# Kernel optimization log

Measured on AMD Instinct MI355X. Metric: run time of the kernel, lower is better.

Reference implementation:

```python
import jax, jax.numpy as jnp
import numpy as np
import math

D_MODEL = 1024
NUM_HEADS = 16
HEAD_DIM = D_MODEL // NUM_HEADS
THETA = 10000.0
B, S = 2, 2048


def _rope(x, positions, theta):
    # x: (b, h, s, d); positions: (s,) int
    d = x.shape[-1]
    inv_freq = theta ** (-jnp.arange(0, d, 2, dtype=jnp.float32) / d)  # (d/2,)
    ang = positions.astype(jnp.float32)[:, None] * inv_freq[None, :]   # (s, d/2)
    cos, sin = jnp.cos(ang), jnp.sin(ang)
    x1 = x[..., ::2]
    x2 = x[..., 1::2]
    r1 = x1 * cos - x2 * sin
    r2 = x1 * sin + x2 * cos
    # interleave back to (..., d)
    return jnp.stack([r1, r2], axis=-1).reshape(x.shape)


def setup_inputs() -> dict:
    key = jax.random.key(0)
    ks = jax.random.split(key, 5)
    std = math.sqrt(2.0 / (D_MODEL + D_MODEL))
    return {
        "x": jax.random.normal(ks[0], (B, S, D_MODEL), dtype=jnp.float32),
        "token_positions": jnp.arange(S, dtype=jnp.int32),
        "Wq": jax.random.normal(ks[1], (D_MODEL, D_MODEL), dtype=jnp.float32) * std,
        "Wk": jax.random.normal(ks[2], (D_MODEL, D_MODEL), dtype=jnp.float32) * std,
        "Wv": jax.random.normal(ks[3], (D_MODEL, D_MODEL), dtype=jnp.float32) * std,
        "Wo": jax.random.normal(ks[4], (D_MODEL, D_MODEL), dtype=jnp.float32) * std,
    }


def reference(x, token_positions, Wq, Wk, Wv, Wo):
    b, s, _ = x.shape
    def split_heads(t):
        return t.reshape(b, s, NUM_HEADS, HEAD_DIM).transpose(0, 2, 1, 3)  # (b,h,s,d)
    Q = split_heads(x @ Wq.T)
    K = split_heads(x @ Wk.T)
    V = split_heads(x @ Wv.T)
    Q = _rope(Q, token_positions, THETA)
    K = _rope(K, token_positions, THETA)
    scores = jnp.einsum("bhqd,bhkd->bhqk", Q, K) / math.sqrt(HEAD_DIM)
    causal = jnp.tril(jnp.ones((s, s), dtype=bool))
    scores = jnp.where(causal, scores, -jnp.inf)
    attn = jax.nn.softmax(scores, axis=-1)
    out = jnp.einsum("bhqk,bhkd->bhqd", attn, V)
    out = out.transpose(0, 2, 1, 3).reshape(b, s, D_MODEL)
    return out @ Wo.T
```

## Files before the change

kernel.cpp:

```cpp
#include <hip/hip_runtime.h>
#include <math.h>

typedef unsigned short u16;
typedef unsigned int   u32;
typedef __attribute__((ext_vector_type(8))) short bf16x8;
typedef __attribute__((ext_vector_type(4))) float floatx4;
typedef __attribute__((ext_vector_type(4))) _Float16 halfx4;
typedef __attribute__((ext_vector_type(2))) unsigned int uintx2;

#define SEQ 2048
#define DM  1024
#define NH  16
#define DH  64
#define MM  4096
#define QSCALE 0.18033688011112042f

__device__ __forceinline__ u16 f2bf(float f) {
    u32 u = __builtin_bit_cast(u32, f);
    u += 0x7fffu + ((u >> 16) & 1u);
    return (u16)(u >> 16);
}

__device__ __forceinline__ void async16(const void* g, void* l) {
    __builtin_amdgcn_global_load_lds(
        (const __attribute__((address_space(1))) void*)g,
        (__attribute__((address_space(3))) void*)l, 16, 0, 0);
}

__global__ __launch_bounds__(256) void prep_kernel(const float* __restrict__ x,
                                                   const float* __restrict__ w0,
                                                   const float* __restrict__ w1,
                                                   const float* __restrict__ w2,
                                                   const float* __restrict__ w3,
                                                   u16* __restrict__ Xsh,
                                                   u16* __restrict__ Wsh,
                                                   const int* __restrict__ pos,
                                                   float2* __restrict__ tab) {
    const int bid = blockIdx.x, cb = blockIdx.y, tid = threadIdx.x;

    int lin = bid * 16 + cb;
    if (lin < 256) {
        int i = lin * 256 + tid;
        int p = i >> 5, d2 = i & 31;
        float freq = __expf(-(float)d2 * (9.2103403719761836f / 32.0f));
        float sv, cv;
        sincosf((float)pos[p] * freq, &sv, &cv);
        tab[i] = make_float2(cv, sv);
    }

    const float* src; u16* dst; int row0;
    if (bid < 64) { src = x; dst = Xsh; row0 = bid * 64; }
    else {
        int wi = (bid - 64) >> 4;
        src = (wi == 0) ? w0 : (wi == 1) ? w1 : (wi == 2) ? w2 : w3;
        dst = Wsh + (size_t)wi * DM * DM;
        row0 = ((bid - 64) & 15) * 64;
    }
    __shared__ __align__(16) u16 t[64 * 64];
#pragma unroll
    for (int rep = 0; rep < 4; ++rep) {
        int f = rep * 256 + tid;
        int r = f >> 4, c4 = f & 15;
        float4 v = *(const float4*)&src[(size_t)(row0 + r) * DM + cb * 64 + c4 * 4];
        uint2 pk;
        pk.x = (u32)f2bf(v.x) | ((u32)f2bf(v.y) << 16);
        pk.y = (u32)f2bf(v.z) | ((u32)f2bf(v.w) << 16);
        int ch = (c4 >> 1) ^ (r & 7);
        *(uint2*)&t[r * 64 + ch * 8 + (c4 & 1) * 4] = pk;
    }
    __syncthreads();
#pragma unroll
    for (int rep = 0; rep < 2; ++rep) {
        int s = rep * 256 + tid;
        int tile = s >> 6, l = s & 63;
        int mt = tile >> 1, kt = tile & 1, lm = l & 15, quad = l >> 4;
        int m = mt * 16 + lm;
        uint4 v = *(const uint4*)&t[m * 64 + ((kt * 4 + quad) ^ (m & 7)) * 8];
        size_t rowblk = (size_t)(row0 >> 4) + mt;
        size_t ktile  = cb * 2 + kt;
        *(uint4*)&dst[(rowblk * 32 + ktile) * 512 + l * 8] = v;
    }
}

template<int NZ, bool OUTF32>
__global__ __launch_bounds__(256, 2) void gemm_f(const u16* __restrict__ Ash,
                                                 const u16* __restrict__ Wbase,
                                                 u16* __restrict__ outbf,
                                                 float* __restrict__ outf,
                                                 _Float16* __restrict__ vtout,
                                                 u16* __restrict__ koutbf,
                                                 const float2* __restrict__ ropetab) {
    const int m0 = blockIdx.x * 64, n0 = blockIdx.y * 128;
    const int tid = threadIdx.x, lane = tid & 63, w = tid >> 6;
    const int lm = lane & 15, quad = lane >> 4;
    const int rb0 = m0 >> 4;
    const int cb0 = n0 >> 4;

    __shared__ __align__(16) u16 lsA[2][4 * 512];
    __shared__ __align__(16) u16 lsB[2][NZ * 8 * 512];

    const u16* aSrc = Ash + ((size_t)(rb0 + w) * 32) * 512 + lane * 8;
    constexpr int NPW = NZ * 2;
    const u16* bSrc[NPW];
#pragma unroll
    for (int j = 0; j < NPW; ++j) {
        int p = w * NPW + j, z = p >> 3, cb8 = p & 7;
        bSrc[j] = Wbase + (size_t)z * (DM * DM)
                + ((size_t)(cb0 + cb8) * 32) * 512 + lane * 8;
    }

    auto stage = [&](int buf, int it) {
        async16(aSrc + (size_t)it * 512, &lsA[buf][w * 512 + lane * 8]);
#pragma unroll
        for (int j = 0; j < NPW; ++j)
            async16(bSrc[j] + (size_t)it * 512,
                    &lsB[buf][(w * NPW + j) * 512 + lane * 8]);
    };

    floatx4 acc[NZ][4][2];
    const floatx4 z4 = {0.f, 0.f, 0.f, 0.f};
#pragma unroll
    for (int z = 0; z < NZ; ++z)
#pragma unroll
        for (int mt = 0; mt < 4; ++mt)
#pragma unroll
            for (int nt = 0; nt < 2; ++nt) acc[z][mt][nt] = z4;

    stage(0, 0);
    __syncthreads();

#pragma unroll 2
    for (int it = 0; it < 32; ++it) {
        if (it < 31) stage((it + 1) & 1, it + 1);
        const u16* La = &lsA[it & 1][0];
        const u16* Lb = &lsB[it & 1][0];
        bf16x8 a[4], b[NZ][2];
#pragma unroll
        for (int mt = 0; mt < 4; ++mt)
            a[mt] = *(const bf16x8*)&La[mt * 512 + lane * 8];
#pragma unroll
        for (int z = 0; z < NZ; ++z)
#pragma unroll
            for (int nt = 0; nt < 2; ++nt)
                b[z][nt] = *(const bf16x8*)&Lb[(z * 8 + w * 2 + nt) * 512 + lane * 8];
#pragma unroll
        for (int z = 0; z < NZ; ++z)
#pragma unroll
            for (int mt = 0; mt < 4; ++mt)
#pragma unroll
                for (int nt = 0; nt < 2; ++nt)
                    acc[z][mt][nt] = __builtin_amdgcn_mfma_f32_16x16x32_bf16(
                        a[mt], b[z][nt], acc[z][mt][nt], 0, 0, 0);
        __syncthreads();
    }

#pragma unroll
    for (int z = 0; z < NZ; ++z) {
        if (!OUTF32 && NZ == 3 && z == 2) {
#pragma unroll
            for (int mt = 0; mt < 4; ++mt) {
                int row = m0 + mt * 16;
                int b = row >> 11;
                int sblk = (row & (SEQ - 1)) >> 4;
#pragma unroll
                for (int nt = 0; nt < 2; ++nt) {
                    int col = n0 + w * 32 + nt * 16;
                    int h = col >> 6;
                    int dblk = (col & 63) >> 4;
                    size_t chunk = ((size_t)(b * NH + h) * 128 + sblk) * 4 + dblk;
                    uint2 pk;
                    pk.x = __builtin_bit_cast(u32, __builtin_amdgcn_cvt_pkrtz(acc[z][mt][nt][0], acc[z][mt][nt][1]));
                    pk.y = __builtin_bit_cast(u32, __builtin_amdgcn_cvt_pkrtz(acc[z][mt][nt][2], acc[z][mt][nt][3]));
                    *(uint2*)&vtout[chunk * 256 + lane * 4] = pk;
                }
            }
            continue;
        }
        if (!OUTF32 && NZ == 3 && z == 1) {
            u16* t = (u16*)&lsB[0][0];
#pragma unroll
            for (int mt = 0; mt < 4; ++mt)
#pragma unroll
                for (int r = 0; r < 4; ++r) {
                    int row = m0 + mt * 16 + quad * 4 + r;
#pragma unroll
                    for (int nt = 0; nt < 2; ++nt) {
                        int col = n0 + w * 32 + nt * 16 + lm;
                        float v  = acc[z][mt][nt][r];
                        float pv = __shfl_xor(v, 1);
                        float2 cs = ropetab[(row & (SEQ - 1)) * 32 + ((col & 63) >> 1)];
                        v = (lm & 1) ? fmaf(pv, cs.y, v * cs.x) : fmaf(v, cs.x, -pv * cs.y);
                        t[(mt * 16 + quad * 4 + r) * 136 + (w * 32 + nt * 16 + lm)] = f2bf(v);
                    }
                }
            __syncthreads();
            {
                int bb = m0 >> 11;
                int sblk0 = (m0 & (SEQ - 1)) >> 4;
                int h0 = n0 >> 6;
#pragma unroll
                for (int j = 0; j < 4; ++j) {
                    int c = w * 4 + j;
                    int hloc = c >> 3, sblkl = (c >> 1) & 3, ks2 = c & 1;
                    uint4 v = *(const uint4*)&t[(sblkl * 16 + lm) * 136 + hloc * 64 + ks2 * 32 + quad * 8];
                    size_t chunk = ((size_t)(bb * NH + h0 + hloc) * 128 + sblk0 + sblkl) * 2 + ks2;
                    *(uint4*)&koutbf[chunk * 512 + lane * 8] = v;
                }
            }
            continue;
        }
        const bool rope = !OUTF32;
        const float osc = (!OUTF32 && z == 0) ? QSCALE : 1.0f;
#pragma unroll
        for (int mt = 0; mt < 4; ++mt)
#pragma unroll
            for (int r = 0; r < 4; ++r) {
                int row = m0 + mt * 16 + quad * 4 + r;
#pragma unroll
                for (int nt = 0; nt < 2; ++nt) {
                    int col = n0 + w * 32 + nt * 16 + lm;
                    float v  = acc[z][mt][nt][r];
                    if (rope) {
                        float pv = __shfl_xor(v, 1);
                        float2 cs = ropetab[(row & (SEQ - 1)) * 32 + ((col & 63) >> 1)];
                        v = (lm & 1) ? fmaf(pv, cs.y, v * cs.x) : fmaf(v, cs.x, -pv * cs.y);
                    }
                    v *= osc;
                    if (OUTF32) {
                        outf[(size_t)row * DM + col] = v;
                    } else {
                        float hv = __shfl_xor(v, 1);
                        if (!(lm & 1)) {
                            u32 pk = (u32)f2bf(v) | ((u32)f2bf(hv) << 16);
                            *(u32*)&outbf[(size_t)z * ((size_t)MM * DM) + (size_t)row * DM + col] = pk;
                        }
                    }
                }
            }
    }
}

__global__ __launch_bounds__(256, 2) void attn_kernel(const u16* __restrict__ Q,
                                                      const u16* __restrict__ Kf,
                                                      const _Float16* __restrict__ Vf,
                                                      u16* __restrict__ AO) {
    const int u  = blockIdx.x;
    const int qt = (u < 256) ? (15 - (u >> 5)) : ((u >> 5) - 8);
    const int bh = u & 31;
    const int b  = bh >> 4, h = bh & 15;
    const int q0 = qt * 128;
    const int tid = threadIdx.x, w = tid >> 6, lane = tid & 63;
    const int lm = lane & 15, quad = lane >> 4;

    __shared__ __align__(16) u16      lsK[2][16 * 512];
    __shared__ __align__(16) _Float16 lsV[2][32 * 256];

    bf16x8 qb[2][2];
#pragma unroll
    for (int qi = 0; qi < 2; ++qi)
#pragma unroll
        for (int ks = 0; ks < 2; ++ks)
            qb[qi][ks] = *(const bf16x8*)
                &Q[(size_t)(b * SEQ + q0 + w * 32 + qi * 16 + lm) * DM + h * DH + ks * 32 + quad * 8];

    const floatx4 z4 = {0.f, 0.f, 0.f, 0.f};
    floatx4 o[2][4];
    floatx4 o5[2];
#pragma unroll
    for (int qi = 0; qi < 2; ++qi) {
#pragma unroll
        for (int dt = 0; dt < 4; ++dt) o[qi][dt] = z4;
        o5[qi] = z4;
    }

    const u16*      Kb = Kf + (size_t)bh * (256 * 512);
    const _Float16* Vb = Vf + (size_t)bh * (128 * 4 * 256);

    auto stageKV = [&](int buf, int kt) {
#pragma unroll
        for (int j = 0; j < 4; ++j) {
            int kc = w * 4 + j;
            async16(Kb + ((size_t)kt * 16 + kc) * 512 + lane * 8,
                    &lsK[buf][kc * 512 + lane * 8]);
            int off = w * 2048 + j * 512 + lane * 8;
            async16(Vb + (size_t)kt * 8192 + off, &lsV[buf][off]);
        }
    };

    stageKV(0, 0);
    const halfx4 ones = {(_Float16)1.f, (_Float16)1.f, (_Float16)1.f, (_Float16)1.f};

    for (int kt = 0; kt <= qt; ++kt) {
        __syncthreads();
        if (kt < qt) stageKV((kt + 1) & 1, kt + 1);
        const u16*      Lk = lsK[kt & 1];
        const _Float16* Lv = lsV[kt & 1];

        floatx4 s4[2][8];
#pragma unroll
        for (int qi = 0; qi < 2; ++qi)
#pragma unroll
            for (int st = 0; st < 8; ++st) s4[qi][st] = z4;
#pragma unroll
        for (int ks = 0; ks < 2; ++ks)
#pragma unroll
            for (int st = 0; st < 8; ++st) {
                bf16x8 ka = *(const bf16x8*)&Lk[(st * 2 + ks) * 512 + lane * 8];
#pragma unroll
                for (int qi = 0; qi < 2; ++qi)
                    s4[qi][st] = __builtin_amdgcn_mfma_f32_16x16x32_bf16(ka, qb[qi][ks], s4[qi][st], 0, 0, 0);
            }

        const bool diag = (kt == qt);
#pragma unroll
        for (int st = 0; st < 8; ++st) {
            halfx4 pb2[2];
#pragma unroll
            for (int qi = 0; qi < 2; ++qi) {
#pragma unroll
                for (int r = 0; r < 4; ++r) {
                    float v = s4[qi][st][r];
                    if (diag) {
                        int keyloc = st * 16 + quad * 4 + r;
                        if (keyloc > w * 32 + qi * 16 + lm) v = -1e30f;
                    }
                    s4[qi][st][r] = exp2f(v);
                }
                uintx2 pk2;
                pk2.x = __builtin_bit_cast(u32, __builtin_amdgcn_cvt_pkrtz(s4[qi][st][0], s4[qi][st][1]));
                pk2.y = __builtin_bit_cast(u32, __builtin_amdgcn_cvt_pkrtz(s4[qi][st][2], s4[qi][st][3]));
                pb2[qi] = __builtin_bit_cast(halfx4, pk2);
            }
#pragma unroll
            for (int dt = 0; dt < 4; ++dt) {
                halfx4 va = *(const halfx4*)&Lv[(st * 4 + dt) * 256 + lane * 4];
#pragma unroll
                for (int qi = 0; qi < 2; ++qi)
                    o[qi][dt] = __builtin_amdgcn_mfma_f32_16x16x16f16(va, pb2[qi], o[qi][dt], 0, 0, 0);
            }
#pragma unroll
            for (int qi = 0; qi < 2; ++qi)
                o5[qi] = __builtin_amdgcn_mfma_f32_16x16x16f16(ones, pb2[qi], o5[qi], 0, 0, 0);
        }
    }

    float rl[2] = {1.0f / o5[0][0], 1.0f / o5[1][0]};

    __syncthreads();
    u16* eb = (u16*)&lsK[0][0];
#pragma unroll
    for (int qi = 0; qi < 2; ++qi) {
        const int q = w * 32 + qi * 16 + lm;
#pragma unroll
        for (int dt = 0; dt < 4; ++dt) {
            uint2 pk;
            pk.x = (u32)f2bf(o[qi][dt][0] * rl[qi]) | ((u32)f2bf(o[qi][dt][1] * rl[qi]) << 16);
            pk.y = (u32)f2bf(o[qi][dt][2] * rl[qi]) | ((u32)f2bf(o[qi][dt][3] * rl[qi]) << 16);
            int ch = (dt * 2 + (quad >> 1)) ^ (lm & 7);
            *(uint2*)&eb[q * 64 + ch * 8 + (quad & 1) * 4] = pk;
        }
    }
    __syncthreads();
    const size_t rowblk0 = (size_t)((b * SEQ + q0) >> 4);
#pragma unroll
    for (int rbi = 0; rbi < 2; ++rbi) {
#pragma unroll
        for (int kt = 0; kt < 2; ++kt) {
            uint4 v = *(const uint4*)&eb[((w * 2 + rbi) * 16 + lm) * 64 + ((kt * 4 + quad) ^ (lm & 7)) * 8];
            *(uint4*)&AO[((rowblk0 + w * 2 + rbi) * 32 + (h * 2 + kt)) * 512 + lane * 8] = v;
        }
    }
}

extern "C" void kernel_launch(void* const* d_in, const int* in_sizes, int n_in,
                              void* d_out, int out_size, void* d_ws, size_t ws_size,
                              hipStream_t stream) {
    const float* x   = (const float*)d_in[0];
    const int*   pos = (const int*)d_in[1];
    float* out = (float*)d_out;

    u16* ws = (u16*)d_ws;
    const size_t MD = (size_t)MM * DM;
    const size_t DD = (size_t)DM * DM;
    u16* Xsh = ws;
    u16* Wsh = ws + MD;
    u16* Qbf = ws + MD + 4 * DD;
    u16* Kfb = Qbf + MD;
    u16* VtB = Kfb + MD;
    float2* ropetab = (float2*)(VtB + MD);
    _Float16* Vt = (_Float16*)VtB;
    u16* AOsh = Xsh;

    prep_kernel<<<dim3(128, 16), 256, 0, stream>>>(
        x, (const float*)d_in[2], (const float*)d_in[3], (const float*)d_in[4],
        (const float*)d_in[5], Xsh, Wsh, pos, ropetab);

    gemm_f<3, false><<<dim3(64, 8), 256, 0, stream>>>(
        Xsh, Wsh, Qbf, nullptr, Vt, Kfb, ropetab);

    attn_kernel<<<dim3(512), 256, 0, stream>>>(Qbf, Kfb, Vt, AOsh);

    gemm_f<1, true><<<dim3(64, 8), 256, 0, stream>>>(
        AOsh, Wsh + 3 * DD, nullptr, out, nullptr, nullptr, ropetab);
}
```

Measured before the change: 185.9 us.

## Split QKV GEMM across grid z and use 128x128 tiles with 2x2 warp layout

Replaces the fused QKV GEMM, which loaded a shared A tile plus three weight tiles per block, with a kernel that handles one projection per blockIdx.z. The QKV tile grows to 128x128 and the output-projection tile to 64x128, with a 2x2 wave arrangement so each wave computes a 64x64 or 32x64 sub-tile. The aim is better register and LDS balance, 3 blocks per CU for the QKV pass, and more balanced MFMA-to-load ratios. In exchange, the X tile is now re-read once per projection instead of being shared across Q, K and V.

Result: faster. 179.5 us (-3.4%).

```diff
diff --git a/kernel.cpp b/kernel.cpp
--- a/kernel.cpp
+++ b/kernel.cpp
@@ -82,49 +82,54 @@
     }
 }
 
-template<int NZ, bool OUTF32>
-__global__ __launch_bounds__(256, 2) void gemm_f(const u16* __restrict__ Ash,
-                                                 const u16* __restrict__ Wbase,
-                                                 u16* __restrict__ outbf,
-                                                 float* __restrict__ outf,
-                                                 _Float16* __restrict__ vtout,
-                                                 u16* __restrict__ koutbf,
-                                                 const float2* __restrict__ ropetab) {
-    const int m0 = blockIdx.x * 64, n0 = blockIdx.y * 128;
+template<int MREP, bool OUTF32>
+__global__ __launch_bounds__(256, (MREP == 4) ? 3 : 2)
+void gemm_s(const u16* __restrict__ Ash,
+            const u16* __restrict__ Wbase,
+            u16* __restrict__ qout,
+            float* __restrict__ outf,
+            _Float16* __restrict__ vtout,
+            u16* __restrict__ kout,
+            const float2* __restrict__ ropetab) {
+    constexpr int BM  = MREP * 32;
+    constexpr int AC  = 2 * MREP;
+    constexpr int APW = AC / 4;
+    constexpr int STEP = (AC + 8) * 512;
+    constexpr int SHN  = (MREP == 4) ? (128 * 136) : (2 * STEP);
+
+    const int z  = blockIdx.z;
+    const u16* Wp = Wbase + (size_t)z * (DM * DM);
+    const int m0 = blockIdx.x * BM, n0 = blockIdx.y * 128;
     const int tid = threadIdx.x, lane = tid & 63, w = tid >> 6;
+    const int wr = w >> 1, wc = w & 1;
     const int lm = lane & 15, quad = lane >> 4;
-    const int rb0 = m0 >> 4;
-    const int cb0 = n0 >> 4;
-
-    __shared__ __align__(16) u16 lsA[2][4 * 512];
-    __shared__ __align__(16) u16 lsB[2][NZ * 8 * 512];
-
-    const u16* aSrc = Ash + ((size_t)(rb0 + w) * 32) * 512 + lane * 8;
-    constexpr int NPW = NZ * 2;
-    const u16* bSrc[NPW];
-#pragma unroll
-    for (int j = 0; j < NPW; ++j) {
-        int p = w * NPW + j, z = p >> 3, cb8 = p & 7;
-        bSrc[j] = Wbase + (size_t)z * (DM * DM)
-                + ((size_t)(cb0 + cb8) * 32) * 512 + lane * 8;
-    }
+    const int rb0 = m0 >> 4, cb0 = n0 >> 4;
+
+    __shared__ __align__(16) u16 sh[SHN];
 
     auto stage = [&](int buf, int it) {
-        async16(aSrc + (size_t)it * 512, &lsA[buf][w * 512 + lane * 8]);
-#pragma unroll
-        for (int j = 0; j < NPW; ++j)
-            async16(bSrc[j] + (size_t)it * 512,
-                    &lsB[buf][(w * NPW + j) * 512 + lane * 8]);
+        u16* la = sh + buf * STEP;
+        u16* lb = la + AC * 512;
+#pragma unroll
+        for (int j = 0; j < APW; ++j) {
+            int c = w * APW + j;
+            async16(Ash + ((size_t)(rb0 + c) * 32 + it) * 512 + lane * 8,
+                    &la[c * 512 + lane * 8]);
+        }
+#pragma unroll
+        for (int j = 0; j < 2; ++j) {
+            int c = w * 2 + j;
+            async16(Wp + ((size_t)(cb0 + c) * 32 + it) * 512 + lane * 8,
+                    &lb[c * 512 + lane * 8]);
+        }
     };
 
-    floatx4 acc[NZ][4][2];
+    floatx4 acc[MREP][4];
     const floatx4 z4 = {0.f, 0.f, 0.f, 0.f};
 #pragma unroll
-    for (int z = 0; z < NZ; ++z)
-#pragma unroll
-        for (int mt = 0; mt < 4; ++mt)
-#pragma unroll
-            for (int nt = 0; nt < 2; ++nt) acc[z][mt][nt] = z4;
+    for (int mt = 0; mt < MREP; ++mt)
+#pragma unroll
+        for (int nt = 0; nt < 4; ++nt) acc[mt][nt] = z4;
 
     stage(0, 0);
     __syncthreads();
@@ -132,111 +137,115 @@
 #pragma unroll 2
     for (int it = 0; it < 32; ++it) {
         if (it < 31) stage((it + 1) & 1, it + 1);
-        const u16* La = &lsA[it & 1][0];
-        const u16* Lb = &lsB[it & 1][0];
-        bf16x8 a[4], b[NZ][2];
-#pragma unroll
-        for (int mt = 0; mt < 4; ++mt)
-            a[mt] = *(const bf16x8*)&La[mt * 512 + lane * 8];
-#pragma unroll
-        for (int z = 0; z < NZ; ++z)
-#pragma unroll
-            for (int nt = 0; nt < 2; ++nt)
-                b[z][nt] = *(const bf16x8*)&Lb[(z * 8 + w * 2 + nt) * 512 + lane * 8];
-#pragma unroll
-        for (int z = 0; z < NZ; ++z)
-#pragma unroll
-            for (int mt = 0; mt < 4; ++mt)
-#pragma unroll
-                for (int nt = 0; nt < 2; ++nt)
-                    acc[z][mt][nt] = __builtin_amdgcn_mfma_f32_16x16x32_bf16(
-                        a[mt], b[z][nt], acc[z][mt][nt], 0, 0, 0);
+        const u16* la = sh + (it & 1) * STEP;
+        const u16* lb = la + AC * 512;
+        bf16x8 a[MREP], b[4];
+#pragma unroll
+        for (int mt = 0; mt < MREP; ++mt)
+            a[mt] = *(const bf16x8*)&la[(wr * MREP + mt) * 512 + lane * 8];
+#pragma unroll
+        for (int nt = 0; nt < 4; ++nt)
+            b[nt] = *(const bf16x8*)&lb[(wc * 4 + nt) * 512 + lane * 8];
+#pragma unroll
+        for (int mt = 0; mt < MREP; ++mt)
+#pragma unroll
+            for (int nt = 0; nt < 4; ++nt)
+                acc[mt][nt] = __builtin_amdgcn_mfma_f32_16x16x32_bf16(
+                    a[mt], b[nt], acc[mt][nt], 0, 0, 0);
         __syncthreads();
     }
 
-#pragma unroll
-    for (int z = 0; z < NZ; ++z) {
-        if (!OUTF32 && NZ == 3 && z == 2) {
-#pragma unroll
-            for (int mt = 0; mt < 4; ++mt) {
-                int row = m0 + mt * 16;
-                int b = row >> 11;
-                int sblk = (row & (SEQ - 1)) >> 4;
-#pragma unroll
-                for (int nt = 0; nt < 2; ++nt) {
-                    int col = n0 + w * 32 + nt * 16;
-                    int h = col >> 6;
-                    int dblk = (col & 63) >> 4;
-                    size_t chunk = ((size_t)(b * NH + h) * 128 + sblk) * 4 + dblk;
-                    uint2 pk;
-                    pk.x = __builtin_bit_cast(u32, __builtin_amdgcn_cvt_pkrtz(acc[z][mt][nt][0], acc[z][mt][nt][1]));
-                    pk.y = __builtin_bit_cast(u32, __builtin_amdgcn_cvt_pkrtz(acc[z][mt][nt][2], acc[z][mt][nt][3]));
-                    *(uint2*)&vtout[chunk * 256 + lane * 4] = pk;
+    if constexpr (OUTF32) {
+#pragma unroll
+        for (int mt = 0; mt < MREP; ++mt)
+#pragma unroll
+            for (int r = 0; r < 4; ++r) {
+                int row = m0 + wr * (MREP * 16) + mt * 16 + quad * 4 + r;
+#pragma unroll
+                for (int nt = 0; nt < 4; ++nt) {
+                    int col = n0 + wc * 64 + nt * 16 + lm;
+                    outf[(size_t)row * DM + col] = acc[mt][nt][r];
                 }
             }
-            continue;
-        }
-        if (!OUTF32 && NZ == 3 && z == 1) {
-            u16* t = (u16*)&lsB[0][0];
-#pragma unroll
-            for (int mt = 0; mt < 4; ++mt)
+        return;
+    } else {
+        if (z == 0) {
+#pragma unroll
+            for (int mt = 0; mt < MREP; ++mt)
 #pragma unroll
                 for (int r = 0; r < 4; ++r) {
-                    int row = m0 + mt * 16 + quad * 4 + r;
-#pragma unroll
-                    for (int nt = 0; nt < 2; ++nt) {
-                        int col = n0 + w * 32 + nt * 16 + lm;
-                        float v  = acc[z][mt][nt][r];
+                    int row = m0 + wr * (MREP * 16) + mt * 16 + quad * 4 + r;
+#pragma unroll
+                    for (int nt = 0; nt < 4; ++nt) {
+                        int col = n0 + wc * 64 + nt * 16 + lm;
+                        float v  = acc[mt][nt][r];
                         float pv = __shfl_xor(v, 1);
                         float2 cs = ropetab[(row & (SEQ - 1)) * 32 + ((col & 63) >> 1)];
                         v = (lm & 1) ? fmaf(pv, cs.y, v * cs.x) : fmaf(v, cs.x, -pv * cs.y);
-                        t[(mt * 16 + quad * 4 + r) * 136 + (w * 32 + nt * 16 + lm)] = f2bf(v);
-                    }
-                }
-            __syncthreads();
-            {
-                int bb = m0 >> 11;
-                int sblk0 = (m0 & (SEQ - 1)) >> 4;
-                int h0 = n0 >> 6;
-#pragma unroll
-                for (int j = 0; j < 4; ++j) {
-                    int c = w * 4 + j;
-                    int hloc = c >> 3, sblkl = (c >> 1) & 3, ks2 = c & 1;
-                    uint4 v = *(const uint4*)&t[(sblkl * 16 + lm) * 136 + hloc * 64 + ks2 * 32 + quad * 8];
-                    size_t chunk = ((size_t)(bb * NH + h0 + hloc) * 128 + sblk0 + sblkl) * 2 + ks2;
-                    *(uint4*)&koutbf[chunk * 512 + lane * 8] = v;
-                }
-            }
-            continue;
-        }
-        const bool rope = !OUTF32;
-        const float osc = (!OUTF32 && z == 0) ? QSCALE : 1.0f;
-#pragma unroll
-        for (int mt = 0; mt < 4; ++mt)
-#pragma unroll
-            for (int r = 0; r < 4; ++r) {
-                int row = m0 + mt * 16 + quad * 4 + r;
-#pragma unroll
-                for (int nt = 0; nt < 2; ++nt) {
-                    int col = n0 + w * 32 + nt * 16 + lm;
-                    float v  = acc[z][mt][nt][r];
-                    if (rope) {
-                        float pv = __shfl_xor(v, 1);
-                        float2 cs = ropetab[(row & (SEQ - 1)) * 32 + ((col & 63) >> 1)];
-                        v = (lm & 1) ? fmaf(pv, cs.y, v * cs.x) : fmaf(v, cs.x, -pv * cs.y);
-                    }
-                    v *= osc;
-                    if (OUTF32) {
-                        outf[(size_t)row * DM + col] = v;
-                    } else {
+                        v *= QSCALE;
                         float hv = __shfl_xor(v, 1);
                         if (!(lm & 1)) {
                             u32 pk = (u32)f2bf(v) | ((u32)f2bf(hv) << 16);
-                            *(u32*)&outbf[(size_t)z * ((size_t)MM * DM) + (size_t)row * DM + col] = pk;
+                            *(u32*)&qout[(size_t)row * DM + col] = pk;
                         }
                     }
                 }
-            }
+        } else if (z == 1) {
+            if constexpr (MREP == 4) {
+                u16* t = sh;
+#pragma unroll
+                for (int mt = 0; mt < MREP; ++mt)
+#pragma unroll
+                    for (int r = 0; r < 4; ++r) {
+                        int rl  = wr * 64 + mt * 16 + quad * 4 + r;
+                        int row = m0 + rl;
+#pragma unroll
+                        for (int nt = 0; nt < 4; ++nt) {
+                            int cl  = wc * 64 + nt * 16 + lm;
+                            int col = n0 + cl;
+                            float v  = acc[mt][nt][r];
+                            float pv = __shfl_xor(v, 1);
+                            float2 cs = ropetab[(row & (SEQ - 1)) * 32 + ((col & 63) >> 1)];
+                            v = (lm & 1) ? fmaf(pv, cs.y, v * cs.x) : fmaf(v, cs.x, -pv * cs.y);
+                            t[rl * 136 + cl] = f2bf(v);
+                        }
+                    }
+                __syncthreads();
+                {
+                    int bb = m0 >> 11;
+                    int sblk0 = (m0 & (SEQ - 1)) >> 4;
+                    int h0 = n0 >> 6;
+#pragma unroll
+                    for (int j = 0; j < 8; ++j) {
+                        int c = w * 8 + j;
+                        int hloc = c >> 4, sblkl = (c >> 1) & 7, ks2 = c & 1;
+                        uint4 v4 = *(const uint4*)&t[(sblkl * 16 + lm) * 136 + hloc * 64 + ks2 * 32 + quad * 8];
+                        size_t chunk = ((size_t)(bb * NH + h0 + hloc) * 128 + sblk0 + sblkl) * 2 + ks2;
+                        *(uint4*)&kout[chunk * 512 + lane * 8] = v4;
+                    }
+                }
+            }
+        } else {
+            if constexpr (MREP == 4) {
+#pragma unroll
+                for (int mt = 0; mt < MREP; ++mt) {
+                    int row = m0 + wr * 64 + mt * 16;
+                    int b = row >> 11;
+                    int sblk = (row & (SEQ - 1)) >> 4;
+#pragma unroll
+                    for (int nt = 0; nt < 4; ++nt) {
+                        int col = n0 + wc * 64 + nt * 16;
+                        int h = col >> 6;
+                        int dblk = (col & 63) >> 4;
+                        size_t chunk = ((size_t)(b * NH + h) * 128 + sblk) * 4 + dblk;
+                        uint2 pk;
+                        pk.x = __builtin_bit_cast(u32, __builtin_amdgcn_cvt_pkrtz(acc[mt][nt][0], acc[mt][nt][1]));
+                        pk.y = __builtin_bit_cast(u32, __builtin_amdgcn_cvt_pkrtz(acc[mt][nt][2], acc[mt][nt][3]));
+                        *(uint2*)&vtout[chunk * 256 + lane * 4] = pk;
+                    }
+                }
+            }
+        }
     }
 }
 
@@ -395,11 +404,11 @@
         x, (const float*)d_in[2], (const float*)d_in[3], (const float*)d_in[4],
         (const float*)d_in[5], Xsh, Wsh, pos, ropetab);
 
-    gemm_f<3, false><<<dim3(64, 8), 256, 0, stream>>>(
+    gemm_s<4, false><<<dim3(32, 8, 3), 256, 0, stream>>>(
         Xsh, Wsh, Qbf, nullptr, Vt, Kfb, ropetab);
 
     attn_kernel<<<dim3(512), 256, 0, stream>>>(Qbf, Kfb, Vt, AOsh);
 
-    gemm_f<1, true><<<dim3(64, 8), 256, 0, stream>>>(
+    gemm_s<2, true><<<dim3(64, 8, 1), 256, 0, stream>>>(
         AOsh, Wsh + 3 * DD, nullptr, out, nullptr, nullptr, ropetab);
 }
```
